# Performance work log

Measured on AMD Instinct MI355X. Metric: run time of the kernel, lower is better.

The kernel has to match this reference:

```python
import jax, jax.numpy as jnp
import numpy as np

N_NODES = 100_000
N_EDGES = 1_600_000
IN_C, HID_C, OUT_C = 128, 64, 32


def gcn_conv(x, W, b, src, dst, n_nodes):
    """PyG GCNConv with add_self_loops=True, symmetric normalization.
    out = D^{-1/2} (A + I) D^{-1/2} (x @ W) + b, with D = deg(A) + 1.
    Self-loop contribution added analytically to avoid materializing loop edges."""
    h = x @ W                                            # [N, F_out]
    deg = jnp.zeros((n_nodes,), h.dtype).at[dst].add(1.0) + 1.0
    dinv = jax.lax.rsqrt(deg)                            # deg >= 1 from self-loops
    norm = dinv[src] * dinv[dst]                         # [E]
    agg = jnp.zeros_like(h).at[dst].add(h[src] * norm[:, None])
    agg = agg + h * (dinv * dinv)[:, None]               # self-loop term
    return agg + b


def setup_inputs() -> dict:
    key = jax.random.key(0)
    ks = jax.random.split(key, 9)
    x = jax.random.normal(ks[0], (N_NODES, IN_C), dtype=jnp.float32)
    edge_index = jax.random.randint(ks[1], (2, N_EDGES), 0, N_NODES, dtype=jnp.int64)
    g = lambda k, fi, fo: jax.random.normal(k, (fi, fo), jnp.float32) * np.sqrt(2.0 / (fi + fo)).astype(np.float32)
    W1 = g(ks[2], IN_C, HID_C)
    b1 = jnp.zeros((HID_C,), jnp.float32)
    W2 = g(ks[3], HID_C, OUT_C)
    b2 = jnp.zeros((OUT_C,), jnp.float32)
    Wl = g(ks[4], IN_C + HID_C + OUT_C, OUT_C)
    bl = jnp.zeros((OUT_C,), jnp.float32)
    return {"x": x, "edge_index": edge_index, "W1": W1, "b1": b1,
            "W2": W2, "b2": b2, "Wl": Wl, "bl": bl}


def reference(x, edge_index, W1, b1, W2, b2, Wl, bl):
    src, dst = edge_index[0], edge_index[1]
    n = x.shape[0]
    h1 = jax.nn.relu(gcn_conv(x, W1, b1, src, dst, n))   # dropout is identity in eval
    h2 = gcn_conv(h1, W2, b2, src, dst, n)
    cat = jnp.concatenate([x, h1, h2], axis=1)           # [N, in+hid+out]
    return jax.nn.log_softmax(cat @ Wl + bl, axis=-1)
```

## Files before the change

kernel.cpp:

```cpp
#include <hip/hip_runtime.h>
#include <hip/hip_bf16.h>

typedef __hip_bfloat16 bf16;
typedef __attribute__((ext_vector_type(8))) short short8;
typedef __attribute__((ext_vector_type(4))) float f32x4;

#define MFMA16(a, b, c) __builtin_amdgcn_mfma_f32_16x16x32_bf16((a), (b), (c), 0, 0, 0)

static __device__ __forceinline__ float ldf(const void* p, long long i, bool f32) {
    return f32 ? ((const float*)p)[i] : __bfloat162float(((const bf16*)p)[i]);
}

static __device__ __forceinline__ short f2bs(float v) {
    union { bf16 h; short s; } u; u.h = __float2bfloat16(v); return u.s;
}

__global__ __launch_bounds__(256, 4)
void sniff_kernel(const void* __restrict__ x, const void* __restrict__ w,
                  const int* __restrict__ ei, int E, int* __restrict__ flags) {
    __shared__ int cnt;
    if (threadIdx.x == 0) cnt = 0;
    __syncthreads();
    if (blockIdx.x < 2) {
        const unsigned short* u = (const unsigned short*)(blockIdx.x == 0 ? x : w);
        int bad = 0;
        for (int i = threadIdx.x; i < 4096; i += 256) {
            unsigned e = (u[i] >> 7) & 0xFF;
            if (e >= 0xA0) bad++;
        }
        atomicAdd(&cnt, bad);
        __syncthreads();
        if (threadIdx.x == 0) flags[blockIdx.x] = (cnt > 16) ? 1 : 0;
    } else {
        int nz = 0;
        for (int i = threadIdx.x; i < 1024; i += 256)
            if (ei[2 * i + 1] != 0) nz++;
        atomicAdd(&cnt, nz);
        __syncthreads();
        if (threadIdx.x == 0) flags[2] = (cnt == 0) ? 1 : 0;
    }
}

static __device__ __forceinline__ int ld_src(const int* ei, int E, int e, bool i64) {
    return i64 ? ei[2 * e] : ei[e];
}
static __device__ __forceinline__ int ld_dst(const int* ei, int E, int e, bool i64) {
    return i64 ? ei[2 * (E + e)] : ei[E + e];
}


__global__ __launch_bounds__(256, 4)
void bhist_kernel(const int* __restrict__ ei, int E, const int* __restrict__ flags,
                  int shift, int NB, int* __restrict__ bucketCount) {
    __shared__ int h[256];
    for (int i = threadIdx.x; i < 256; i += 256) h[i] = 0;
    __syncthreads();
    bool i64 = flags[2] != 0;
    int base = blockIdx.x * 4096;
    for (int i = 0; i < 16; i++) {
        int e = base + i * 256 + threadIdx.x;
        if (e < E) atomicAdd(&h[ld_dst(ei, E, e, i64) >> shift], 1);
    }
    __syncthreads();
    for (int i = threadIdx.x; i < NB; i += 256)
        if (h[i]) atomicAdd(&bucketCount[i], h[i]);
}

__global__ __launch_bounds__(256, 4)
void bscan_kernel(const int* __restrict__ bucketCount, int NB,
                  int* __restrict__ bucketBase, int* __restrict__ bcursor, int E) {
    __shared__ int bs[256];
    int v = ((int)threadIdx.x < NB) ? bucketCount[threadIdx.x] : 0;
    bs[threadIdx.x] = v;
    __syncthreads();
    for (int off = 1; off < 256; off <<= 1) {
        int t = ((int)threadIdx.x >= off) ? bs[threadIdx.x - off] : 0;
        __syncthreads();
        bs[threadIdx.x] += t;
        __syncthreads();
    }
    int excl = bs[threadIdx.x] - v;
    if ((int)threadIdx.x < NB) { bucketBase[threadIdx.x] = excl; bcursor[threadIdx.x] = excl; }
    if (threadIdx.x == 0) bucketBase[NB] = E;
}

__global__ __launch_bounds__(256, 4)
void bpart_kernel(const int* __restrict__ ei, int E, const int* __restrict__ flags,
                  int shift, int NB, int* __restrict__ bcursor, int2* __restrict__ ebuf) {
    __shared__ int h[256];
    __shared__ int gofs[256];
    for (int i = threadIdx.x; i < 256; i += 256) h[i] = 0;
    __syncthreads();
    bool i64 = flags[2] != 0;
    int base = blockIdx.x * 4096;
    for (int i = 0; i < 16; i++) {
        int e = base + i * 256 + threadIdx.x;
        if (e < E) atomicAdd(&h[ld_dst(ei, E, e, i64) >> shift], 1);
    }
    __syncthreads();
    if ((int)threadIdx.x < NB) {
        int c = h[threadIdx.x];
        gofs[threadIdx.x] = c ? atomicAdd(&bcursor[threadIdx.x], c) : 0;
    }
    __syncthreads();
    for (int i = threadIdx.x; i < 256; i += 256) h[i] = 0;
    __syncthreads();
    for (int i = 0; i < 16; i++) {
        int e = base + i * 256 + threadIdx.x;
        if (e < E) {
            int s = ld_src(ei, E, e, i64), d = ld_dst(ei, E, e, i64);
            int b = d >> shift;
            int p = atomicAdd(&h[b], 1);
            ebuf[gofs[b] + p] = make_int2(s, d);
        }
    }
}

__global__ __launch_bounds__(256, 2)
void bbuild_kernel(const int2* __restrict__ ebuf, const int* __restrict__ bucketBase,
                   int shift, int N, int E, int* __restrict__ rowptr,
                   float* __restrict__ dinv, int* __restrict__ csr_src) {
    __shared__ int cnt[1024];
    __shared__ int exc[1024];
    __shared__ int bs[256];
    int b = blockIdx.x;
    int nodeBase = b << shift;
    int width = 1 << shift;
    int nn = N - nodeBase; if (nn > width) nn = width;
    int beg = bucketBase[b], end = bucketBase[b + 1];
    for (int i = threadIdx.x; i < width; i += 256) cnt[i] = 0;
    __syncthreads();
    for (int e = beg + threadIdx.x; e < end; e += 256)
        atomicAdd(&cnt[ebuf[e].y - nodeBase], 1);
    __syncthreads();
    int per = width / 256;
    int s = 0;
    int base4 = threadIdx.x * per;
    for (int i = 0; i < per; i++) s += cnt[base4 + i];
    bs[threadIdx.x] = s;
    __syncthreads();
    for (int off = 1; off < 256; off <<= 1) {
        int t = ((int)threadIdx.x >= off) ? bs[threadIdx.x - off] : 0;
        __syncthreads();
        bs[threadIdx.x] += t;
        __syncthreads();
    }
    int run = bs[threadIdx.x] - s;
    for (int i = 0; i < per; i++) { exc[base4 + i] = run; run += cnt[base4 + i]; }
    __syncthreads();
    for (int i = threadIdx.x; i < nn; i += 256) {
        int node = nodeBase + i;
        rowptr[node] = beg + exc[i];
        dinv[node] = rsqrtf((float)cnt[i] + 1.0f);
    }
    __syncthreads();
    for (int i = threadIdx.x; i < width; i += 256) cnt[i] = 0;
    __syncthreads();
    for (int e = beg + threadIdx.x; e < end; e += 256) {
        int2 v = ebuf[e];
        int l = v.y - nodeBase;
        int p = atomicAdd(&cnt[l], 1);
        csr_src[beg + exc[l] + p] = v.x;
    }
    if (b == 0 && threadIdx.x == 0) rowptr[N] = E;
}

__global__ __launch_bounds__(256, 4)
void repack_kernel(const void* __restrict__ W1, const void* __restrict__ W2,
                   const void* __restrict__ Wl, const int* __restrict__ flags,
                   bf16* __restrict__ Bp1, bf16* __restrict__ Bp2, bf16* __restrict__ Bp3) {
    bool fw = flags[1] != 0;
    const void* W; bf16* Bp; int ntiles, nc, nfrag;
    if (blockIdx.x == 0)      { W = W1; Bp = Bp1; ntiles = 4; nc = 64; nfrag = 16; }
    else if (blockIdx.x == 1) { W = W2; Bp = Bp2; ntiles = 2; nc = 32; nfrag = 4;  }
    else                      { W = Wl; Bp = Bp3; ntiles = 2; nc = 32; nfrag = 14; }
    for (int s = threadIdx.x; s < nfrag * 64; s += 256) {
        int f = s >> 6, lane = s & 63;
        int kstep = f / ntiles, ntile = f % ntiles;
        int n = ntile * 16 + (lane & 15);
        int kbase = kstep * 32 + (lane >> 4) * 8;
#pragma unroll
        for (int j = 0; j < 8; j++)
            Bp[s * 8 + j] = __float2bfloat16(ldf(W, (long long)(kbase + j) * nc + n, fw));
    }
}

__global__ __launch_bounds__(256, 4)
void cvt_x_kernel(const void* __restrict__ x, const int* __restrict__ flags,
                  short* __restrict__ xb, long long total8) {
    long long i = (long long)blockIdx.x * 256 + threadIdx.x;
    if (i >= total8) return;
    bool fx = flags[0] != 0;
    short8 o;
    if (fx) {
        const float4* xf = (const float4*)x;
        float4 a = xf[i * 2], b = xf[i * 2 + 1];
        o[0] = f2bs(a.x); o[1] = f2bs(a.y); o[2] = f2bs(a.z); o[3] = f2bs(a.w);
        o[4] = f2bs(b.x); o[5] = f2bs(b.y); o[6] = f2bs(b.z); o[7] = f2bs(b.w);
    } else {
        o = ((const short8*)x)[i];
    }
    ((short8*)xb)[i] = o;
}

__global__ __launch_bounds__(256, 3)
void gemm1_mfma_kernel(const short* __restrict__ xb, const bf16* __restrict__ Bpack,
                       float* __restrict__ h1x, int N) {
    int lane = threadIdx.x & 63, wave = threadIdx.x >> 6;
    int m = lane & 15, quad = lane >> 4;
    int base = blockIdx.x * 128 + wave * 32;
    if (base >= N) return;
    const short8* bp = (const short8*)Bpack;
    short8 B[16];
#pragma unroll
    for (int i = 0; i < 16; i++) B[i] = bp[i * 64 + lane];
    if (base + 32 <= N) {
#pragma unroll
        for (int t = 0; t < 2; t++) {
            int r0 = base + t * 16;
            const short* xr = &xb[(long long)(r0 + m) * 128 + quad * 8];
            short8 A[4];
#pragma unroll
            for (int k = 0; k < 4; k++) A[k] = *(const short8*)(xr + k * 32);
            f32x4 acc[4];
#pragma unroll
            for (int nt = 0; nt < 4; nt++) acc[nt] = (f32x4){0.f, 0.f, 0.f, 0.f};
#pragma unroll
            for (int k = 0; k < 4; k++) {
#pragma unroll
                for (int nt = 0; nt < 4; nt++) acc[nt] = MFMA16(A[k], B[k * 4 + nt], acc[nt]);
            }
            float* o = &h1x[(long long)(r0 + quad * 4) * 64 + m];
#pragma unroll
            for (int nt = 0; nt < 4; nt++) {
#pragma unroll
                for (int r = 0; r < 4; r++) o[(long long)r * 64 + nt * 16] = acc[nt][r];
            }
        }
    } else {
#pragma unroll
        for (int t = 0; t < 2; t++) {
            int r0 = base + t * 16;
            int row = r0 + m;
            short8 A[4];
#pragma unroll
            for (int k = 0; k < 4; k++) A[k] = (short8){0,0,0,0,0,0,0,0};
            if (row < N) {
                const short* xr = &xb[(long long)row * 128 + quad * 8];
#pragma unroll
                for (int k = 0; k < 4; k++) A[k] = *(const short8*)(xr + k * 32);
            }
            f32x4 acc[4];
#pragma unroll
            for (int nt = 0; nt < 4; nt++) acc[nt] = (f32x4){0.f, 0.f, 0.f, 0.f};
#pragma unroll
            for (int k = 0; k < 4; k++) {
#pragma unroll
                for (int nt = 0; nt < 4; nt++) acc[nt] = MFMA16(A[k], B[k * 4 + nt], acc[nt]);
            }
#pragma unroll
            for (int r = 0; r < 4; r++) {
                int orow = r0 + quad * 4 + r;
                if (orow < N) {
                    float* o = &h1x[(long long)orow * 64 + m];
#pragma unroll
                    for (int nt = 0; nt < 4; nt++) o[nt * 16] = acc[nt][r];
                }
            }
        }
    }
}

__global__ __launch_bounds__(256, 8)
void gather1_kernel(const float* __restrict__ h1x, const float* __restrict__ dinv,
                    const int* __restrict__ rowptr, const int* __restrict__ csr_src,
                    const void* __restrict__ b1, const int* __restrict__ flags,
                    bf16* __restrict__ h1b, int N) {
    bool fw = flags[1] != 0;
    int lane = threadIdx.x & 63;
    int node = blockIdx.x * 4 + (threadIdx.x >> 6);
    if (node >= N) return;
    int beg = rowptr[node], end = rowptr[node + 1];
    float dvd = dinv[node];
    float acc = 0.f;
    for (int b = beg; b < end; b += 64) {
        int cnt = end - b; if (cnt > 64) cnt = 64;
        int s = 0; float dvs = 0.f;
        if (lane < cnt) { s = csr_src[b + lane]; dvs = dinv[s]; }
        for (int j = 0; j < cnt; j += 8) {
            int sj[8]; float nm[8];
#pragma unroll
            for (int u = 0; u < 8; u++) {
                int idx = j + u;
                int sel = (idx < cnt) ? idx : 0;
                sj[u] = __shfl(s, sel);
                float w = __shfl(dvs, sel) * dvd;
                nm[u] = (idx < cnt) ? w : 0.f;
            }
            float v[8];
#pragma unroll
            for (int u = 0; u < 8; u++) v[u] = h1x[(long long)sj[u] * 64 + lane];
#pragma unroll
            for (int u = 0; u < 8; u++) acc = fmaf(v[u], nm[u], acc);
        }
    }
    float v = acc + h1x[(long long)node * 64 + lane] * (dvd * dvd) + ldf(b1, lane, fw);
    h1b[(long long)node * 64 + lane] = __float2bfloat16(fmaxf(v, 0.f));
}

__global__ __launch_bounds__(256, 4)
void gemm2_mfma_kernel(const short* __restrict__ h1b, const bf16* __restrict__ Bpack,
                       float* __restrict__ h2x, int N) {
    int lane = threadIdx.x & 63, wave = threadIdx.x >> 6;
    int m = lane & 15, quad = lane >> 4;
    int r0 = blockIdx.x * 64 + wave * 16;
    if (r0 >= N) return;
    const short8* bp = (const short8*)Bpack;
    short8 B[4];
#pragma unroll
    for (int i = 0; i < 4; i++) B[i] = bp[i * 64 + lane];
    f32x4 acc0 = {0.f,0.f,0.f,0.f}, acc1 = {0.f,0.f,0.f,0.f};
    if (r0 + 16 <= N) {
        const short* xr = &h1b[(long long)(r0 + m) * 64 + quad * 8];
#pragma unroll
        for (int k = 0; k < 2; k++) {
            short8 A = *(const short8*)(xr + k * 32);
            acc0 = MFMA16(A, B[k * 2 + 0], acc0);
            acc1 = MFMA16(A, B[k * 2 + 1], acc1);
        }
        float* o = &h2x[(long long)(r0 + quad * 4) * 32 + m];
#pragma unroll
        for (int r = 0; r < 4; r++) { o[(long long)r * 32] = acc0[r]; o[(long long)r * 32 + 16] = acc1[r]; }
    } else {
        int row = r0 + m;
#pragma unroll
        for (int k = 0; k < 2; k++) {
            short8 A = {0,0,0,0,0,0,0,0};
            if (row < N) A = *(const short8*)&h1b[(long long)row * 64 + k * 32 + quad * 8];
            acc0 = MFMA16(A, B[k * 2 + 0], acc0);
            acc1 = MFMA16(A, B[k * 2 + 1], acc1);
        }
#pragma unroll
        for (int r = 0; r < 4; r++) {
            int orow = r0 + quad * 4 + r;
            if (orow < N) {
                h2x[(long long)orow * 32 + m] = acc0[r];
                h2x[(long long)orow * 32 + 16 + m] = acc1[r];
            }
        }
    }
}

__global__ __launch_bounds__(256, 8)
void gather2_kernel(const float* __restrict__ h2x, const float* __restrict__ dinv,
                    const int* __restrict__ rowptr, const int* __restrict__ csr_src,
                    const void* __restrict__ b2, const int* __restrict__ flags,
                    bf16* __restrict__ h2b, int N) {
    bool fw = flags[1] != 0;
    int j = threadIdx.x & 31;
    int node = blockIdx.x * 8 + (threadIdx.x >> 5);
    if (node >= N) return;
    int beg = rowptr[node], end = rowptr[node + 1];
    float dvd = dinv[node];
    float acc = 0.f;
    for (int b = beg; b < end; b += 32) {
        int cnt = end - b; if (cnt > 32) cnt = 32;
        int s = 0; float dvs = 0.f;
        if (j < cnt) { s = csr_src[b + j]; dvs = dinv[s]; }
        for (int jj = 0; jj < cnt; jj += 8) {
            int sj[8]; float nm[8];
#pragma unroll
            for (int u = 0; u < 8; u++) {
                int idx = jj + u;
                int sel = (idx < cnt) ? idx : 0;
                sj[u] = __shfl(s, sel, 32);
                float w = __shfl(dvs, sel, 32) * dvd;
                nm[u] = (idx < cnt) ? w : 0.f;
            }
            float v[8];
#pragma unroll
            for (int u = 0; u < 8; u++) v[u] = h2x[(long long)sj[u] * 32 + j];
#pragma unroll
            for (int u = 0; u < 8; u++) acc = fmaf(v[u], nm[u], acc);
        }
    }
    acc += h2x[(long long)node * 32 + j] * (dvd * dvd) + ldf(b2, j, fw);
    h2b[(long long)node * 32 + j] = __float2bfloat16(acc);
}

__global__ __launch_bounds__(256, 2)
void final_mfma_kernel(const short* __restrict__ xb, const short* __restrict__ h1b,
                       const short* __restrict__ h2b, const bf16* __restrict__ Bpack,
                       const void* __restrict__ bl, const int* __restrict__ flags,
                       void* __restrict__ out, int N) {
    bool fw = flags[1] != 0, fx = flags[0] != 0;
    int lane = threadIdx.x & 63, wave = threadIdx.x >> 6;
    int m = lane & 15, quad = lane >> 4;
    int r0 = blockIdx.x * 64 + wave * 16;
    if (r0 >= N) return;
    const short8* bp = (const short8*)Bpack;
    short8 B[14];
#pragma unroll
    for (int i = 0; i < 14; i++) B[i] = bp[i * 64 + lane];
    f32x4 acc0 = {0.f,0.f,0.f,0.f}, acc1 = {0.f,0.f,0.f,0.f};
    bool full = (r0 + 16 <= N);
    int row = r0 + m;
    bool rowok = full || (row < N);
#pragma unroll
    for (int s = 0; s < 7; s++) {
        short8 A = {0,0,0,0,0,0,0,0};
        if (rowok) {
            const short* p;
            if (s < 4)      p = &xb [(long long)row * 128 + s * 32 + quad * 8];
            else if (s < 6) p = &h1b[(long long)row * 64 + (s - 4) * 32 + quad * 8];
            else            p = &h2b[(long long)row * 32 + quad * 8];
            A = *(const short8*)p;
        }
        acc0 = MFMA16(A, B[s * 2 + 0], acc0);
        acc1 = MFMA16(A, B[s * 2 + 1], acc1);
    }
    float bl0 = ldf(bl, m, fw), bl1 = ldf(bl, m + 16, fw);
#pragma unroll
    for (int r = 0; r < 4; r++) {
        float v0 = acc0[r] + bl0, v1 = acc1[r] + bl1;
        float mx = fmaxf(v0, v1);
#pragma unroll
        for (int o = 8; o > 0; o >>= 1) mx = fmaxf(mx, __shfl_xor(mx, o));
        float sm = __expf(v0 - mx) + __expf(v1 - mx);
#pragma unroll
        for (int o = 8; o > 0; o >>= 1) sm += __shfl_xor(sm, o);
        float lse = mx + __logf(sm);
        int orow = r0 + quad * 4 + r;
        if (orow < N) {
            if (fx) {
                ((float*)out)[(long long)orow * 32 + m]      = v0 - lse;
                ((float*)out)[(long long)orow * 32 + 16 + m] = v1 - lse;
            } else {
                ((bf16*)out)[(long long)orow * 32 + m]      = __float2bfloat16(v0 - lse);
                ((bf16*)out)[(long long)orow * 32 + 16 + m] = __float2bfloat16(v1 - lse);
            }
        }
    }
}

extern "C" void kernel_launch(void* const* d_in, const int* in_sizes, int n_in,
                              void* d_out, int out_size, void* d_ws, size_t ws_size,
                              hipStream_t stream) {
    const void* x  = d_in[0];
    const int*  ei = (const int*)d_in[1];
    const void* W1 = d_in[2];
    const void* b1 = d_in[3];
    const void* W2 = d_in[4];
    const void* b2 = d_in[5];
    const void* Wl = d_in[6];
    const void* bl = d_in[7];

    int N = in_sizes[0] / 128;
    int E = in_sizes[1] / 2;

    int shift = 9;
    while (((N + (1 << shift) - 1) >> shift) > 256 && shift < 10) shift++;
    int NB = (N + (1 << shift) - 1) >> shift;

    int* ip      = (int*)d_ws;
    int* flags   = ip;
    int* bucketCount = ip + 16;
    int* bucketBase  = bucketCount + 256;
    int* bcursor     = bucketBase + 272;
    float* dinv  = (float*)(bcursor + 256);
    int* rowptr  = (int*)(dinv + N);
    bf16* Bp1    = (bf16*)(rowptr + N + 16);
    bf16* Bp2    = (bf16*)((int*)Bp1 + 4096);
    bf16* Bp3    = (bf16*)((int*)Bp2 + 1024);
    int* csr_src = (int*)Bp3 + 3584;
    short* xb    = (short*)(csr_src + E);
    int*   Ai    = (int*)xb + (size_t)N * 64;
    int2*  ebuf  = (int2*)Ai;
    float* h1x   = (float*)Ai;
    float* h2x   = (float*)Ai;
    bf16*  h2b   = (bf16*)(Ai + (size_t)N * 48);
    bf16*  h1b   = (bf16*)(Ai + (size_t)N * 64);

    hipMemsetAsync(ip, 0, (16 + 256) * sizeof(int), stream);

    sniff_kernel<<<3, 256, 0, stream>>>(x, W1, ei, E, flags);

    int nchunk = (E + 4095) / 4096;
    bhist_kernel<<<nchunk, 256, 0, stream>>>(ei, E, flags, shift, NB, bucketCount);
    bscan_kernel<<<1, 256, 0, stream>>>(bucketCount, NB, bucketBase, bcursor, E);
    bpart_kernel<<<nchunk, 256, 0, stream>>>(ei, E, flags, shift, NB, bcursor, ebuf);
    bbuild_kernel<<<NB, 256, 0, stream>>>(ebuf, bucketBase, shift, N, E, rowptr, dinv, csr_src);

    repack_kernel<<<3, 256, 0, stream>>>(W1, W2, Wl, flags, Bp1, Bp2, Bp3);

    long long total8 = (long long)N * 16;
    cvt_x_kernel<<<(int)((total8 + 255) / 256), 256, 0, stream>>>(x, flags, xb, total8);

    gemm1_mfma_kernel<<<(N + 127) / 128, 256, 0, stream>>>(xb, Bp1, h1x, N);
    gather1_kernel<<<(N + 3) / 4, 256, 0, stream>>>(h1x, dinv, rowptr, csr_src, b1, flags, h1b, N);
    gemm2_mfma_kernel<<<(N + 63) / 64, 256, 0, stream>>>((const short*)h1b, Bp2, h2x, N);
    gather2_kernel<<<(N + 7) / 8, 256, 0, stream>>>(h2x, dinv, rowptr, csr_src, b2, flags, h2b, N);
    final_mfma_kernel<<<(N + 63) / 64, 256, 0, stream>>>(xb, (const short*)h1b, (const short*)h2b,
                                                         Bp3, bl, flags, d_out, N);
}
```

Baseline: 343.9 us.

## Fold source-side dinv into GEMM epilogues and simplify gather kernels

The GEMM epilogues now scale each output row by dinv[row], so the gathers only sum pre-scaled neighbor rows and multiply once by dinv[dst]. That removes the per-edge dinv[src] load and the shuffle-based normalization. The gathers read csr_src with uniform scalar loads, 16 edges per iteration. gather2 now uses a full 64-lane wave per node with two half-waves splitting the edges, combined by an xor shuffle. This cuts dependent loads and shuffle work per edge, at the cost of redundant index loads for masked tail iterations.

After: 347.2 us. No clear change (+0.9%).

```diff
diff --git a/kernel.cpp b/kernel.cpp
--- a/kernel.cpp
+++ b/kernel.cpp
@@ -205,7 +205,7 @@
 
 __global__ __launch_bounds__(256, 3)
 void gemm1_mfma_kernel(const short* __restrict__ xb, const bf16* __restrict__ Bpack,
-                       float* __restrict__ h1x, int N) {
+                       const float* __restrict__ dinv, float* __restrict__ h1g, int N) {
     int lane = threadIdx.x & 63, wave = threadIdx.x >> 6;
     int m = lane & 15, quad = lane >> 4;
     int base = blockIdx.x * 128 + wave * 32;
@@ -230,11 +230,14 @@
 #pragma unroll
                 for (int nt = 0; nt < 4; nt++) acc[nt] = MFMA16(A[k], B[k * 4 + nt], acc[nt]);
             }
-            float* o = &h1x[(long long)(r0 + quad * 4) * 64 + m];
+            float dv[4];
+#pragma unroll
+            for (int r = 0; r < 4; r++) dv[r] = dinv[r0 + quad * 4 + r];
+            float* o = &h1g[(long long)(r0 + quad * 4) * 64 + m];
 #pragma unroll
             for (int nt = 0; nt < 4; nt++) {
 #pragma unroll
-                for (int r = 0; r < 4; r++) o[(long long)r * 64 + nt * 16] = acc[nt][r];
+                for (int r = 0; r < 4; r++) o[(long long)r * 64 + nt * 16] = acc[nt][r] * dv[r];
             }
         }
     } else {
@@ -262,9 +265,10 @@
             for (int r = 0; r < 4; r++) {
                 int orow = r0 + quad * 4 + r;
                 if (orow < N) {
-                    float* o = &h1x[(long long)orow * 64 + m];
-#pragma unroll
-                    for (int nt = 0; nt < 4; nt++) o[nt * 16] = acc[nt][r];
+                    float dv = dinv[orow];
+                    float* o = &h1g[(long long)orow * 64 + m];
+#pragma unroll
+                    for (int nt = 0; nt < 4; nt++) o[nt * 16] = acc[nt][r] * dv;
                 }
             }
         }
@@ -272,45 +276,39 @@
 }
 
 __global__ __launch_bounds__(256, 8)
-void gather1_kernel(const float* __restrict__ h1x, const float* __restrict__ dinv,
+void gather1_kernel(const float* __restrict__ h1g, const float* __restrict__ dinv,
                     const int* __restrict__ rowptr, const int* __restrict__ csr_src,
                     const void* __restrict__ b1, const int* __restrict__ flags,
                     bf16* __restrict__ h1b, int N) {
     bool fw = flags[1] != 0;
     int lane = threadIdx.x & 63;
-    int node = blockIdx.x * 4 + (threadIdx.x >> 6);
+    int wv = __builtin_amdgcn_readfirstlane(threadIdx.x >> 6);
+    int node = blockIdx.x * 4 + wv;
     if (node >= N) return;
     int beg = rowptr[node], end = rowptr[node + 1];
     float dvd = dinv[node];
+    const float* hL = h1g + lane;
     float acc = 0.f;
-    for (int b = beg; b < end; b += 64) {
-        int cnt = end - b; if (cnt > 64) cnt = 64;
-        int s = 0; float dvs = 0.f;
-        if (lane < cnt) { s = csr_src[b + lane]; dvs = dinv[s]; }
-        for (int j = 0; j < cnt; j += 8) {
-            int sj[8]; float nm[8];
-#pragma unroll
-            for (int u = 0; u < 8; u++) {
-                int idx = j + u;
-                int sel = (idx < cnt) ? idx : 0;
-                sj[u] = __shfl(s, sel);
-                float w = __shfl(dvs, sel) * dvd;
-                nm[u] = (idx < cnt) ? w : 0.f;
-            }
-            float v[8];
-#pragma unroll
-            for (int u = 0; u < 8; u++) v[u] = h1x[(long long)sj[u] * 64 + lane];
-#pragma unroll
-            for (int u = 0; u < 8; u++) acc = fmaf(v[u], nm[u], acc);
-        }
-    }
-    float v = acc + h1x[(long long)node * 64 + lane] * (dvd * dvd) + ldf(b1, lane, fw);
-    h1b[(long long)node * 64 + lane] = __float2bfloat16(fmaxf(v, 0.f));
+    for (int b = beg; b < end; b += 16) {
+        float v[16], m[16];
+#pragma unroll
+        for (int u = 0; u < 16; u++) {
+            int i = b + u;
+            int s = csr_src[(i < end) ? i : beg];
+            m[u] = (i < end) ? 1.f : 0.f;
+            v[u] = hL[(long long)s * 64];
+        }
+#pragma unroll
+        for (int u = 0; u < 16; u++) acc = fmaf(v[u], m[u], acc);
+    }
+    float gs = h1g[(long long)node * 64 + lane];
+    float o = dvd * (acc + gs) + ldf(b1, lane, fw);
+    h1b[(long long)node * 64 + lane] = __float2bfloat16(fmaxf(o, 0.f));
 }
 
 __global__ __launch_bounds__(256, 4)
 void gemm2_mfma_kernel(const short* __restrict__ h1b, const bf16* __restrict__ Bpack,
-                       float* __restrict__ h2x, int N) {
+                       const float* __restrict__ dinv, float* __restrict__ h2g, int N) {
     int lane = threadIdx.x & 63, wave = threadIdx.x >> 6;
     int m = lane & 15, quad = lane >> 4;
     int r0 = blockIdx.x * 64 + wave * 16;
@@ -328,9 +326,15 @@
             acc0 = MFMA16(A, B[k * 2 + 0], acc0);
             acc1 = MFMA16(A, B[k * 2 + 1], acc1);
         }
-        float* o = &h2x[(long long)(r0 + quad * 4) * 32 + m];
-#pragma unroll
-        for (int r = 0; r < 4; r++) { o[(long long)r * 32] = acc0[r]; o[(long long)r * 32 + 16] = acc1[r]; }
+        float dv[4];
+#pragma unroll
+        for (int r = 0; r < 4; r++) dv[r] = dinv[r0 + quad * 4 + r];
+        float* o = &h2g[(long long)(r0 + quad * 4) * 32 + m];
+#pragma unroll
+        for (int r = 0; r < 4; r++) {
+            o[(long long)r * 32] = acc0[r] * dv[r];
+            o[(long long)r * 32 + 16] = acc1[r] * dv[r];
+        }
     } else {
         int row = r0 + m;
 #pragma unroll
@@ -344,48 +348,51 @@
         for (int r = 0; r < 4; r++) {
             int orow = r0 + quad * 4 + r;
             if (orow < N) {
-                h2x[(long long)orow * 32 + m] = acc0[r];
-                h2x[(long long)orow * 32 + 16 + m] = acc1[r];
+                float dv = dinv[orow];
+                h2g[(long long)orow * 32 + m] = acc0[r] * dv;
+                h2g[(long long)orow * 32 + 16 + m] = acc1[r] * dv;
             }
         }
     }
 }
 
 __global__ __launch_bounds__(256, 8)
-void gather2_kernel(const float* __restrict__ h2x, const float* __restrict__ dinv,
+void gather2_kernel(const float* __restrict__ h2g, const float* __restrict__ dinv,
                     const int* __restrict__ rowptr, const int* __restrict__ csr_src,
                     const void* __restrict__ b2, const int* __restrict__ flags,
                     bf16* __restrict__ h2b, int N) {
     bool fw = flags[1] != 0;
-    int j = threadIdx.x & 31;
-    int node = blockIdx.x * 8 + (threadIdx.x >> 5);
+    int lane = threadIdx.x & 63;
+    int ch = lane & 31, half = lane >> 5;
+    int wv = __builtin_amdgcn_readfirstlane(threadIdx.x >> 6);
+    int node = blockIdx.x * 4 + wv;
     if (node >= N) return;
     int beg = rowptr[node], end = rowptr[node + 1];
     float dvd = dinv[node];
+    const float* hL = h2g + ch;
     float acc = 0.f;
-    for (int b = beg; b < end; b += 32) {
-        int cnt = end - b; if (cnt > 32) cnt = 32;
-        int s = 0; float dvs = 0.f;
-        if (j < cnt) { s = csr_src[b + j]; dvs = dinv[s]; }
-        for (int jj = 0; jj < cnt; jj += 8) {
-            int sj[8]; float nm[8];
-#pragma unroll
-            for (int u = 0; u < 8; u++) {
-                int idx = jj + u;
-                int sel = (idx < cnt) ? idx : 0;
-                sj[u] = __shfl(s, sel, 32);
-                float w = __shfl(dvs, sel, 32) * dvd;
-                nm[u] = (idx < cnt) ? w : 0.f;
-            }
-            float v[8];
-#pragma unroll
-            for (int u = 0; u < 8; u++) v[u] = h2x[(long long)sj[u] * 32 + j];
-#pragma unroll
-            for (int u = 0; u < 8; u++) acc = fmaf(v[u], nm[u], acc);
-        }
-    }
-    acc += h2x[(long long)node * 32 + j] * (dvd * dvd) + ldf(b2, j, fw);
-    h2b[(long long)node * 32 + j] = __float2bfloat16(acc);
+    for (int b = beg; b < end; b += 16) {
+        float v[8], m[8];
+#pragma unroll
+        for (int u = 0; u < 8; u++) {
+            int i0 = b + 2 * u, i1 = i0 + 1;
+            int s0 = csr_src[(i0 < end) ? i0 : beg];
+            int s1 = csr_src[(i1 < end) ? i1 : beg];
+            float m0 = (i0 < end) ? 1.f : 0.f;
+            float m1 = (i1 < end) ? 1.f : 0.f;
+            int s = half ? s1 : s0;
+            m[u] = half ? m1 : m0;
+            v[u] = hL[(long long)s * 32];
+        }
+#pragma unroll
+        for (int u = 0; u < 8; u++) acc = fmaf(v[u], m[u], acc);
+    }
+    acc += __shfl_xor(acc, 32);
+    if (half == 0) {
+        float gs = h2g[(long long)node * 32 + ch];
+        float o = dvd * (acc + gs) + ldf(b2, ch, fw);
+        h2b[(long long)node * 32 + ch] = __float2bfloat16(o);
+    }
 }
 
 __global__ __launch_bounds__(256, 2)
@@ -476,8 +483,8 @@
     short* xb    = (short*)(csr_src + E);
     int*   Ai    = (int*)xb + (size_t)N * 64;
     int2*  ebuf  = (int2*)Ai;
-    float* h1x   = (float*)Ai;
-    float* h2x   = (float*)Ai;
+    float* h1g   = (float*)Ai;
+    float* h2g   = (float*)Ai;
     bf16*  h2b   = (bf16*)(Ai + (size_t)N * 48);
     bf16*  h1b   = (bf16*)(Ai + (size_t)N * 64);
 
@@ -496,10 +503,10 @@
     long long total8 = (long long)N * 16;
     cvt_x_kernel<<<(int)((total8 + 255) / 256), 256, 0, stream>>>(x, flags, xb, total8);
 
-    gemm1_mfma_kernel<<<(N + 127) / 128, 256, 0, stream>>>(xb, Bp1, h1x, N);
-    gather1_kernel<<<(N + 3) / 4, 256, 0, stream>>>(h1x, dinv, rowptr, csr_src, b1, flags, h1b, N);
-    gemm2_mfma_kernel<<<(N + 63) / 64, 256, 0, stream>>>((const short*)h1b, Bp2, h2x, N);
-    gather2_kernel<<<(N + 7) / 8, 256, 0, stream>>>(h2x, dinv, rowptr, csr_src, b2, flags, h2b, N);
+    gemm1_mfma_kernel<<<(N + 127) / 128, 256, 0, stream>>>(xb, Bp1, dinv, h1g, N);
+    gather1_kernel<<<(N + 3) / 4, 256, 0, stream>>>(h1g, dinv, rowptr, csr_src, b1, flags, h1b, N);
+    gemm2_mfma_kernel<<<(N + 63) / 64, 256, 0, stream>>>((const short*)h1b, Bp2, dinv, h2g, N);
+    gather2_kernel<<<(N + 3) / 4, 256, 0, stream>>>(h2g, dinv, rowptr, csr_src, b2, flags, h2b, N);
     final_mfma_kernel<<<(N + 63) / 64, 256, 0, stream>>>(xb, (const short*)h1b, (const short*)h2b,
                                                          Bp3, bl, flags, d_out, N);
 }
```
